# Kernel optimization log

Hardware: AMD Instinct MI355X
Metric: run time of the kernel (lower is better)

## Reference

```python
import jax, jax.numpy as jnp
import numpy as np

N = 128       # batch (hard-coded in the torch module)
NEG = 112     # negatives per anchor (N - 16 per-class samples)
HALF = 56
MARGIN = 0.3
EPS = 1e-12
D = 2048


def _pair_dist(x, y):
    xx = jnp.sum(x * x, axis=1, keepdims=True)          # [m,1]
    yy = jnp.sum(y * y, axis=1, keepdims=True).T        # [1,n]
    d2 = xx + yy - 2.0 * (x @ y.T)
    return jnp.sqrt(jnp.maximum(d2, EPS))


def _row_dist(a, b):
    # diagonal of euclidean_dist(a, b): per-row distance, same clamp/sqrt
    d2 = jnp.sum(a * a, axis=1) + jnp.sum(b * b, axis=1) - 2.0 * jnp.sum(a * b, axis=1)
    return jnp.sqrt(jnp.maximum(d2, EPS))


def setup_inputs() -> dict:
    key = jax.random.key(0)
    k1, k2 = jax.random.split(key)
    global_feat1 = jax.random.normal(k1, (N, D), dtype=jnp.float32)
    global_feat2 = jax.random.normal(k2, (N, D), dtype=jnp.float32)
    # PK-sampled labels: 8 identities x 8 samples, duplicated across two modalities
    # -> exactly 16 positives / 112 negatives per anchor (required by the hard-coded views)
    labels = jnp.repeat(jnp.arange(8, dtype=jnp.int64), 8)
    target = jnp.tile(labels, 2)  # [128]
    return {"global_feat1": global_feat1, "global_feat2": global_feat2, "target": target}


def reference(global_feat1, global_feat2, target):
    dist_mat = _pair_dist(global_feat1, global_feat2)           # [N,N]
    is_pos = target[None, :] == target[:, None]                 # [N,N]

    # hard_example_mining: hardest positive / hardest negative per anchor
    dist_ap = jnp.max(jnp.where(is_pos, dist_mat, -jnp.inf), axis=1)  # [N]

    # negative column indices per row, in ascending column order (matches
    # torch boolean-mask row-major flattening). Stable argsort: False (neg) first.
    neg_idx = jnp.argsort(is_pos.astype(jnp.int32), axis=1, stable=True)[:, :NEG]  # [N,112]
    dist_neg = jnp.take_along_axis(dist_mat, neg_idx, axis=1)                      # [N,112]

    # per-row top-1 smallest negative in each 56-half (the 128-iter torch loop)
    i1 = jnp.argmin(dist_neg[:, :HALF], axis=1)          # [N]
    i2 = jnp.argmin(dist_neg[:, HALF:], axis=1) + HALF   # [N]
    r = jnp.arange(N)
    sel1 = neg_idx[r, i1]
    sel2 = neg_idx[r, i2]
    # mean of the two selected hard negatives (features taken from global_feat1)
    feat_mean = 0.5 * (global_feat1[sel1] + global_feat1[sel2])  # [N,D]

    c0, c1, c2, c3 = jnp.split(feat_mean, 4, axis=0)
    feat_rgb_mid = jnp.concatenate([c0, c2], axis=0)             # [64,D]
    feat_ir_mid = jnp.concatenate([c1, c3], axis=0)              # [64,D]

    H = N // 2
    feat_rgb = jnp.concatenate([global_feat1[:H], global_feat2[:H]], axis=0)  # [128,D]
    feat_ir = jnp.concatenate([global_feat1[H:], global_feat2[H:]], axis=0)   # [128,D]

    # torch.diag of a [128,64] matrix keeps only the first 64 diagonal entries
    d_rgb = _row_dist(feat_rgb[:64], feat_rgb_mid)   # [64]
    d_ir = _row_dist(feat_ir[:64], feat_ir_mid)      # [64]
    dist_an = jnp.concatenate([d_rgb, d_ir], axis=0)  # [128]

    triplets = dist_ap - dist_an + MARGIN
    pos_mask = triplets > 0
    loss = jnp.sum(jnp.where(pos_mask, triplets, 0.0)) / 128.0
    num_active = jnp.sum(pos_mask.astype(jnp.int32))
    return loss, num_active
```

## Files before the change

kernel.cpp:

```cpp
#include <hip/hip_runtime.h>
#include <math.h>

#define NN 128
#define DD 2048
#define LDSTR 132

__device__ __forceinline__ float waveReduceSum(float v) {
#pragma unroll
  for (int o = 32; o > 0; o >>= 1) v += __shfl_down(v, o, 64);
  return v;
}

__global__ __launch_bounds__(256) void k_gram(const float* __restrict__ f1,
                                              const float* __restrict__ f2,
                                              float* __restrict__ ctrl,
                                              float* __restrict__ dbuf,
                                              int split) {
  __shared__ float s1[32 * LDSTR];
  __shared__ float s2[32 * LDSTR];
  const int t = threadIdx.x;

  if (blockIdx.x == 0 && blockIdx.y == 0 && blockIdx.z == 0 && t == 0) {
    ctrl[0] = 0.f;
    ctrl[1] = 0.f;
    ((unsigned*)ctrl)[2] = 0u;
  }

  const int i0 = blockIdx.x * 32;
  const int j0 = blockIdx.y * 32;
  const int kc = blockIdx.z * 128;

  {
    const int row = t >> 3;
    const int c0 = (t & 7) * 4;
    const float* p1 = f1 + (size_t)(i0 + row) * DD + kc;
    const float* p2 = f2 + (size_t)(j0 + row) * DD + kc;
#pragma unroll
    for (int u = 0; u < 4; ++u) {
      const int c = c0 + 32 * u;
      *(float4*)&s1[row * LDSTR + c] = *(const float4*)(p1 + c);
      *(float4*)&s2[row * LDSTR + c] = *(const float4*)(p2 + c);
    }
  }
  __syncthreads();

  const int ii = t >> 4;
  const int jj = t & 15;
  float a00 = 0.f, a01 = 0.f, a10 = 0.f, a11 = 0.f;

#pragma unroll 4
  for (int k = 0; k < 128; k += 4) {
    float4 x0 = *(const float4*)&s1[ii * LDSTR + k];
    float4 x1 = *(const float4*)&s1[(ii + 16) * LDSTR + k];
    float4 y0 = *(const float4*)&s2[jj * LDSTR + k];
    float4 y1 = *(const float4*)&s2[(jj + 16) * LDSTR + k];
#define STEP(C)                                          \
    {                                                    \
      float d0 = x0.C - y0.C; a00 = fmaf(d0, d0, a00);   \
      float d1 = x0.C - y1.C; a01 = fmaf(d1, d1, a01);   \
      float d2v = x1.C - y0.C; a10 = fmaf(d2v, d2v, a10);\
      float d3 = x1.C - y1.C; a11 = fmaf(d3, d3, a11);   \
    }
    STEP(x) STEP(y) STEP(z) STEP(w)
#undef STEP
  }

  const int ia = i0 + ii, ib = i0 + ii + 16;
  const int ja = j0 + jj, jb = j0 + jj + 16;
  if (split) {
    float* dst = dbuf + (size_t)blockIdx.z * NN * NN;
    dst[ia * NN + ja] = a00;
    dst[ia * NN + jb] = a01;
    dst[ib * NN + ja] = a10;
    dst[ib * NN + jb] = a11;
  } else {
    atomicAdd(&dbuf[ia * NN + ja], a00);
    atomicAdd(&dbuf[ia * NN + jb], a01);
    atomicAdd(&dbuf[ib * NN + ja], a10);
    atomicAdd(&dbuf[ib * NN + jb], a11);
  }
}

__global__ __launch_bounds__(256) void k_mine_an(const float* __restrict__ f1,
                                                 float* __restrict__ ctrl,
                                                 const float* __restrict__ dbuf,
                                                 float* __restrict__ out,
                                                 int split) {
  const int k = blockIdx.x;
  int m = k;
  if (k >= 32 && k < 64) m = k + 32;
  else if (k >= 64 && k < 96) m = k - 32;

  const int t = threadIdx.x;
  const int lane = t & 63;
  const int wv = t >> 6;
  const int j = t & 127;

  __shared__ unsigned long long sg0[2], sg1[2];
  __shared__ float spos[2];
  __shared__ int ssel[2];
  __shared__ float sap;
  __shared__ float sred[4];

  const int rrow = (t < 128) ? m : k;
  float v;
  if (split) {
    float s = 0.f;
#pragma unroll
    for (int p = 0; p < 16; ++p) s += dbuf[p * NN * NN + rrow * NN + j];
    v = s;
  } else {
    v = dbuf[rrow * NN + j];
  }

  if (t < 128) {
    const int L8 = ((m & 63) >> 3) * 8;
    const bool isneg = (((j & 63) >> 3) != ((m & 63) >> 3));
    int c1 = j - L8;        c1 = c1 < 0 ? 0 : (c1 > 8 ? 8 : c1);
    int c2 = j - (64 + L8); c2 = c2 < 0 ? 0 : (c2 > 8 ? 8 : c2);
    const int negc = j - c1 - c2;
    const unsigned long long key =
        ((unsigned long long)__float_as_uint(v) << 32) | (unsigned)j;
    unsigned long long k0 = (isneg && negc < 56) ? key : ~0ull;
    unsigned long long k1 = (isneg && negc >= 56) ? key : ~0ull;
#pragma unroll
    for (int o = 32; o > 0; o >>= 1) {
      unsigned long long o0 = __shfl_down(k0, o, 64);
      unsigned long long o1 = __shfl_down(k1, o, 64);
      k0 = o0 < k0 ? o0 : k0;
      k1 = o1 < k1 ? o1 : k1;
    }
    if (lane == 0) { sg0[wv] = k0; sg1[wv] = k1; }
  } else {
    const bool ispos = (((j & 63) >> 3) == ((k & 63) >> 3));
    float pv = ispos ? v : -1.f;
#pragma unroll
    for (int o = 32; o > 0; o >>= 1) pv = fmaxf(pv, __shfl_down(pv, o, 64));
    if (lane == 0) spos[wv - 2] = pv;
  }
  __syncthreads();
  if (t == 0) {
    const unsigned long long b0 = sg0[0] < sg0[1] ? sg0[0] : sg0[1];
    const unsigned long long b1 = sg1[0] < sg1[1] ? sg1[0] : sg1[1];
    ssel[0] = (int)(unsigned)(b0 & 0xffffffffu);
    ssel[1] = (int)(unsigned)(b1 & 0xffffffffu);
    const float apv = fmaxf(spos[0], spos[1]);
    sap = sqrtf(fmaxf(apv, 1e-12f));
  }
  __syncthreads();

  const int a = ssel[0], b = ssel[1];
  const float4* pk = (const float4*)(f1 + (size_t)k * DD);
  const float4* pa = (const float4*)(f1 + (size_t)a * DD);
  const float4* pb = (const float4*)(f1 + (size_t)b * DD);
  float acc = 0.f;
#pragma unroll
  for (int it = 0; it < 2; ++it) {
    const int idx = it * 256 + t;
    float4 xk = pk[idx];
    float4 xa = pa[idx];
    float4 xb = pb[idx];
    float d;
    d = xk.x - 0.5f * (xa.x + xb.x); acc = fmaf(d, d, acc);
    d = xk.y - 0.5f * (xa.y + xb.y); acc = fmaf(d, d, acc);
    d = xk.z - 0.5f * (xa.z + xb.z); acc = fmaf(d, d, acc);
    d = xk.w - 0.5f * (xa.w + xb.w); acc = fmaf(d, d, acc);
  }
  acc = waveReduceSum(acc);
  if (lane == 0) sred[wv] = acc;
  __syncthreads();
  if (t == 0) {
    const float d2v = sred[0] + sred[1] + sred[2] + sred[3];
    const float dan = sqrtf(fmaxf(d2v, 1e-12f));
    const float trip = sap - dan + 0.3f;
    const float pos = trip > 0.f ? trip : 0.f;
    const float act = trip > 0.f ? 1.f : 0.f;
    atomicAdd(&ctrl[0], pos);
    atomicAdd(&ctrl[1], act);
    __threadfence();
    const unsigned tk = __hip_atomic_fetch_add((unsigned*)ctrl + 2, 1u,
                                               __ATOMIC_ACQ_REL,
                                               __HIP_MEMORY_SCOPE_AGENT);
    if (tk == NN - 1) {
      const float ls = __hip_atomic_load(&ctrl[0], __ATOMIC_RELAXED,
                                         __HIP_MEMORY_SCOPE_AGENT);
      const float ct = __hip_atomic_load(&ctrl[1], __ATOMIC_RELAXED,
                                         __HIP_MEMORY_SCOPE_AGENT);
      out[0] = ls * (1.f / 128.f);
      out[1] = ct;
    }
  }
}

extern "C" void kernel_launch(void* const* d_in, const int* in_sizes, int n_in,
                              void* d_out, int out_size, void* d_ws, size_t ws_size,
                              hipStream_t stream) {
  const float* f1 = (const float*)d_in[0];
  const float* f2 = (const float*)d_in[1];

  float* ws = (float*)d_ws;
  float* ctrl = ws;
  float* dbuf = ws + 16;

  const bool split = ws_size >= (size_t)16 * NN * NN * sizeof(float) + 64;
  if (!split) {
    hipMemsetAsync(dbuf, 0, NN * NN * sizeof(float), stream);
  }

  k_gram<<<dim3(4, 4, 16), 256, 0, stream>>>(f1, f2, ctrl, dbuf, (int)split);
  k_mine_an<<<NN, 256, 0, stream>>>(f1, ctrl, dbuf, (float*)d_out, (int)split);
}
```

Measured before the change: 68.99 us.

## Fuse distance computation with mining into one per-anchor kernel, deterministic finish

Replaces the tiled split-K distance kernel plus the mining kernel with one 1024-thread block per anchor. Each block computes only the row distances it needs (128 negative-row entries for the permuted row m and 16 positive entries for k) directly from global memory, with the anchor rows cached in LDS. A small second kernel reduces the per-anchor triplets, replacing the atomic counter and ticket scheme. This removes the 16-way partial buffer write/read and the inter-kernel dependency on the full matrix, but each block now streams f2 (about 1 MB) on its own, so total traffic rises and relies on L2 reuse.

```diff
diff --git a/kernel.cpp b/kernel.cpp
--- a/kernel.cpp
+++ b/kernel.cpp
@@ -3,7 +3,6 @@
 
 #define NN 128
 #define DD 2048
-#define LDSTR 132
 
 __device__ __forceinline__ float waveReduceSum(float v) {
 #pragma unroll
@@ -11,81 +10,9 @@
   return v;
 }
 
-__global__ __launch_bounds__(256) void k_gram(const float* __restrict__ f1,
-                                              const float* __restrict__ f2,
-                                              float* __restrict__ ctrl,
-                                              float* __restrict__ dbuf,
-                                              int split) {
-  __shared__ float s1[32 * LDSTR];
-  __shared__ float s2[32 * LDSTR];
-  const int t = threadIdx.x;
-
-  if (blockIdx.x == 0 && blockIdx.y == 0 && blockIdx.z == 0 && t == 0) {
-    ctrl[0] = 0.f;
-    ctrl[1] = 0.f;
-    ((unsigned*)ctrl)[2] = 0u;
-  }
-
-  const int i0 = blockIdx.x * 32;
-  const int j0 = blockIdx.y * 32;
-  const int kc = blockIdx.z * 128;
-
-  {
-    const int row = t >> 3;
-    const int c0 = (t & 7) * 4;
-    const float* p1 = f1 + (size_t)(i0 + row) * DD + kc;
-    const float* p2 = f2 + (size_t)(j0 + row) * DD + kc;
-#pragma unroll
-    for (int u = 0; u < 4; ++u) {
-      const int c = c0 + 32 * u;
-      *(float4*)&s1[row * LDSTR + c] = *(const float4*)(p1 + c);
-      *(float4*)&s2[row * LDSTR + c] = *(const float4*)(p2 + c);
-    }
-  }
-  __syncthreads();
-
-  const int ii = t >> 4;
-  const int jj = t & 15;
-  float a00 = 0.f, a01 = 0.f, a10 = 0.f, a11 = 0.f;
-
-#pragma unroll 4
-  for (int k = 0; k < 128; k += 4) {
-    float4 x0 = *(const float4*)&s1[ii * LDSTR + k];
-    float4 x1 = *(const float4*)&s1[(ii + 16) * LDSTR + k];
-    float4 y0 = *(const float4*)&s2[jj * LDSTR + k];
-    float4 y1 = *(const float4*)&s2[(jj + 16) * LDSTR + k];
-#define STEP(C)                                          \
-    {                                                    \
-      float d0 = x0.C - y0.C; a00 = fmaf(d0, d0, a00);   \
-      float d1 = x0.C - y1.C; a01 = fmaf(d1, d1, a01);   \
-      float d2v = x1.C - y0.C; a10 = fmaf(d2v, d2v, a10);\
-      float d3 = x1.C - y1.C; a11 = fmaf(d3, d3, a11);   \
-    }
-    STEP(x) STEP(y) STEP(z) STEP(w)
-#undef STEP
-  }
-
-  const int ia = i0 + ii, ib = i0 + ii + 16;
-  const int ja = j0 + jj, jb = j0 + jj + 16;
-  if (split) {
-    float* dst = dbuf + (size_t)blockIdx.z * NN * NN;
-    dst[ia * NN + ja] = a00;
-    dst[ia * NN + jb] = a01;
-    dst[ib * NN + ja] = a10;
-    dst[ib * NN + jb] = a11;
-  } else {
-    atomicAdd(&dbuf[ia * NN + ja], a00);
-    atomicAdd(&dbuf[ia * NN + jb], a01);
-    atomicAdd(&dbuf[ib * NN + ja], a10);
-    atomicAdd(&dbuf[ib * NN + jb], a11);
-  }
-}
-
-__global__ __launch_bounds__(256) void k_mine_an(const float* __restrict__ f1,
-                                                 float* __restrict__ ctrl,
-                                                 const float* __restrict__ dbuf,
-                                                 float* __restrict__ out,
-                                                 int split) {
+__global__ __launch_bounds__(1024) void k_fused(const float* __restrict__ f1,
+                                                const float* __restrict__ f2,
+                                                float* __restrict__ trips) {
   const int k = blockIdx.x;
   int m = k;
   if (k >= 32 && k < 64) m = k + 32;
@@ -93,102 +20,130 @@
 
   const int t = threadIdx.x;
   const int lane = t & 63;
-  const int wv = t >> 6;
-  const int j = t & 127;
+  const int w = t >> 6;
 
-  __shared__ unsigned long long sg0[2], sg1[2];
-  __shared__ float spos[2];
+  __shared__ float sm[DD];
+  __shared__ float sk[DD];
+  __shared__ float snd[NN];
+  __shared__ float spd[16];
   __shared__ int ssel[2];
   __shared__ float sap;
-  __shared__ float sred[4];
+  __shared__ float sred[16];
 
-  const int rrow = (t < 128) ? m : k;
-  float v;
-  if (split) {
-    float s = 0.f;
+  if (t < 512) {
+    ((float4*)sm)[t] = ((const float4*)(f1 + (size_t)m * DD))[t];
+  } else {
+    ((float4*)sk)[t - 512] = ((const float4*)(f1 + (size_t)k * DD))[t - 512];
+  }
+  __syncthreads();
+
 #pragma unroll
-    for (int p = 0; p < 16; ++p) s += dbuf[p * NN * NN + rrow * NN + j];
-    v = s;
-  } else {
-    v = dbuf[rrow * NN + j];
+  for (int c = 0; c < 8; ++c) {
+    const int j = w * 8 + c;
+    const float4* __restrict__ p2 = (const float4*)(f2 + (size_t)j * DD);
+    float acc = 0.f;
+#pragma unroll
+    for (int q = 0; q < 8; ++q) {
+      const int idx = lane + 64 * q;
+      const float4 y = p2[idx];
+      const float4 x = ((const float4*)sm)[idx];
+      float d;
+      d = x.x - y.x; acc = fmaf(d, d, acc);
+      d = x.y - y.y; acc = fmaf(d, d, acc);
+      d = x.z - y.z; acc = fmaf(d, d, acc);
+      d = x.w - y.w; acc = fmaf(d, d, acc);
+    }
+    acc = waveReduceSum(acc);
+    if (lane == 0) snd[j] = acc;
   }
 
-  if (t < 128) {
-    const int L8 = ((m & 63) >> 3) * 8;
-    const bool isneg = (((j & 63) >> 3) != ((m & 63) >> 3));
-    int c1 = j - L8;        c1 = c1 < 0 ? 0 : (c1 > 8 ? 8 : c1);
-    int c2 = j - (64 + L8); c2 = c2 < 0 ? 0 : (c2 > 8 ? 8 : c2);
-    const int negc = j - c1 - c2;
-    const unsigned long long key =
-        ((unsigned long long)__float_as_uint(v) << 32) | (unsigned)j;
-    unsigned long long k0 = (isneg && negc < 56) ? key : ~0ull;
-    unsigned long long k1 = (isneg && negc >= 56) ? key : ~0ull;
+  {
+    const int L8k = ((k & 63) >> 3) * 8;
+    const int j = (w < 8) ? (L8k + w) : (64 + L8k + (w - 8));
+    const float4* __restrict__ p2 = (const float4*)(f2 + (size_t)j * DD);
+    float acc = 0.f;
+#pragma unroll
+    for (int q = 0; q < 8; ++q) {
+      const int idx = lane + 64 * q;
+      const float4 y = p2[idx];
+      const float4 x = ((const float4*)sk)[idx];
+      float d;
+      d = x.x - y.x; acc = fmaf(d, d, acc);
+      d = x.y - y.y; acc = fmaf(d, d, acc);
+      d = x.z - y.z; acc = fmaf(d, d, acc);
+      d = x.w - y.w; acc = fmaf(d, d, acc);
+    }
+    acc = waveReduceSum(acc);
+    if (lane == 0) spd[w] = acc;
+  }
+  __syncthreads();
+
+  if (w == 0) {
+    const int lm = (m & 63) >> 3;
+    const bool isneg = ((lane >> 3) != lm);
+    const float v0 = snd[lane];
+    const float v1 = snd[lane + 64];
+    unsigned long long k0 = isneg
+        ? (((unsigned long long)__float_as_uint(v0) << 32) | (unsigned)lane)
+        : ~0ull;
+    unsigned long long k1 = isneg
+        ? (((unsigned long long)__float_as_uint(v1) << 32) | (unsigned)(lane + 64))
+        : ~0ull;
 #pragma unroll
     for (int o = 32; o > 0; o >>= 1) {
-      unsigned long long o0 = __shfl_down(k0, o, 64);
-      unsigned long long o1 = __shfl_down(k1, o, 64);
+      const unsigned long long o0 = __shfl_down(k0, o, 64);
+      const unsigned long long o1 = __shfl_down(k1, o, 64);
       k0 = o0 < k0 ? o0 : k0;
       k1 = o1 < k1 ? o1 : k1;
     }
-    if (lane == 0) { sg0[wv] = k0; sg1[wv] = k1; }
-  } else {
-    const bool ispos = (((j & 63) >> 3) == ((k & 63) >> 3));
-    float pv = ispos ? v : -1.f;
+    if (lane == 0) {
+      ssel[0] = (int)(unsigned)(k0 & 0xffffffffu);
+      ssel[1] = (int)(unsigned)(k1 & 0xffffffffu);
+    }
+  } else if (t == 64) {
+    float ap = spd[0];
 #pragma unroll
-    for (int o = 32; o > 0; o >>= 1) pv = fmaxf(pv, __shfl_down(pv, o, 64));
-    if (lane == 0) spos[wv - 2] = pv;
-  }
-  __syncthreads();
-  if (t == 0) {
-    const unsigned long long b0 = sg0[0] < sg0[1] ? sg0[0] : sg0[1];
-    const unsigned long long b1 = sg1[0] < sg1[1] ? sg1[0] : sg1[1];
-    ssel[0] = (int)(unsigned)(b0 & 0xffffffffu);
-    ssel[1] = (int)(unsigned)(b1 & 0xffffffffu);
-    const float apv = fmaxf(spos[0], spos[1]);
-    sap = sqrtf(fmaxf(apv, 1e-12f));
+    for (int i = 1; i < 16; ++i) ap = fmaxf(ap, spd[i]);
+    sap = sqrtf(fmaxf(ap, 1e-12f));
   }
   __syncthreads();
 
   const int a = ssel[0], b = ssel[1];
-  const float4* pk = (const float4*)(f1 + (size_t)k * DD);
-  const float4* pa = (const float4*)(f1 + (size_t)a * DD);
-  const float4* pb = (const float4*)(f1 + (size_t)b * DD);
-  float acc = 0.f;
-#pragma unroll
-  for (int it = 0; it < 2; ++it) {
-    const int idx = it * 256 + t;
-    float4 xk = pk[idx];
-    float4 xa = pa[idx];
-    float4 xb = pb[idx];
-    float d;
-    d = xk.x - 0.5f * (xa.x + xb.x); acc = fmaf(d, d, acc);
-    d = xk.y - 0.5f * (xa.y + xb.y); acc = fmaf(d, d, acc);
-    d = xk.z - 0.5f * (xa.z + xb.z); acc = fmaf(d, d, acc);
-    d = xk.w - 0.5f * (xa.w + xb.w); acc = fmaf(d, d, acc);
+  {
+    const float2 xa = ((const float2*)(f1 + (size_t)a * DD))[t];
+    const float2 xb = ((const float2*)(f1 + (size_t)b * DD))[t];
+    const float2 xk = ((const float2*)sk)[t];
+    float d = xk.x - 0.5f * (xa.x + xb.x);
+    float acc = d * d;
+    d = xk.y - 0.5f * (xa.y + xb.y);
+    acc = fmaf(d, d, acc);
+    acc = waveReduceSum(acc);
+    if (lane == 0) sred[w] = acc;
   }
-  acc = waveReduceSum(acc);
-  if (lane == 0) sred[wv] = acc;
   __syncthreads();
   if (t == 0) {
-    const float d2v = sred[0] + sred[1] + sred[2] + sred[3];
+    float d2v = 0.f;
+#pragma unroll
+    for (int i = 0; i < 16; ++i) d2v += sred[i];
     const float dan = sqrtf(fmaxf(d2v, 1e-12f));
-    const float trip = sap - dan + 0.3f;
-    const float pos = trip > 0.f ? trip : 0.f;
-    const float act = trip > 0.f ? 1.f : 0.f;
-    atomicAdd(&ctrl[0], pos);
-    atomicAdd(&ctrl[1], act);
-    __threadfence();
-    const unsigned tk = __hip_atomic_fetch_add((unsigned*)ctrl + 2, 1u,
-                                               __ATOMIC_ACQ_REL,
-                                               __HIP_MEMORY_SCOPE_AGENT);
-    if (tk == NN - 1) {
-      const float ls = __hip_atomic_load(&ctrl[0], __ATOMIC_RELAXED,
-                                         __HIP_MEMORY_SCOPE_AGENT);
-      const float ct = __hip_atomic_load(&ctrl[1], __ATOMIC_RELAXED,
-                                         __HIP_MEMORY_SCOPE_AGENT);
-      out[0] = ls * (1.f / 128.f);
-      out[1] = ct;
-    }
+    trips[k] = sap - dan + 0.3f;
+  }
+}
+
+__global__ __launch_bounds__(128) void k_finish(const float* __restrict__ trips,
+                                                float* __restrict__ out) {
+  const int t = threadIdx.x;
+  const float tr = trips[t];
+  float pos = tr > 0.f ? tr : 0.f;
+  float act = tr > 0.f ? 1.f : 0.f;
+  pos = waveReduceSum(pos);
+  act = waveReduceSum(act);
+  __shared__ float sp[2], sa[2];
+  if ((t & 63) == 0) { sp[t >> 6] = pos; sa[t >> 6] = act; }
+  __syncthreads();
+  if (t == 0) {
+    out[0] = (sp[0] + sp[1]) * (1.f / 128.f);
+    out[1] = sa[0] + sa[1];
   }
 }
 
@@ -197,16 +152,7 @@
                               hipStream_t stream) {
   const float* f1 = (const float*)d_in[0];
   const float* f2 = (const float*)d_in[1];
-
-  float* ws = (float*)d_ws;
-  float* ctrl = ws;
-  float* dbuf = ws + 16;
-
-  const bool split = ws_size >= (size_t)16 * NN * NN * sizeof(float) + 64;
-  if (!split) {
-    hipMemsetAsync(dbuf, 0, NN * NN * sizeof(float), stream);
-  }
-
-  k_gram<<<dim3(4, 4, 16), 256, 0, stream>>>(f1, f2, ctrl, dbuf, (int)split);
-  k_mine_an<<<NN, 256, 0, stream>>>(f1, ctrl, dbuf, (float*)d_out, (int)split);
+  float* trips = (float*)d_ws;
+  k_fused<<<NN, 1024, 0, stream>>>(f1, f2, trips);
+  k_finish<<<1, 128, 0, stream>>>(trips, (float*)d_out);
 }
```

Result: slower. 71.06 us (+3.0%).
